# Kernel tuning notes

Measured on AMD Instinct MI355X. Metric: run time of the kernel, lower is better.

The kernel has to match this reference:

```python
import jax, jax.numpy as jnp
import numpy as np
from jax import lax

SLOPE = 0.01  # nn.LeakyReLU default negative slope

def leaky(x):
    return jnp.where(x >= 0, x, SLOPE * x)

def conv2d(x, w, b, pad):
    # x: [N,C,H,W], w: [O,I,kh,kw]
    y = lax.conv_general_dilated(x, w, (1, 1), [(pad, pad), (pad, pad)],
                                 dimension_numbers=('NCHW', 'OIHW', 'NCHW'))
    return y + b[None, :, None, None]

def centered_ifftn(x, axes):
    # np.fft.fftshift(np.fft.ifftn(np.fft.ifftshift(X), norm='ortho'))
    return jnp.fft.fftshift(jnp.fft.ifftn(jnp.fft.ifftshift(x, axes=axes), axes=axes, norm='ortho'), axes=axes)

def setup_inputs() -> dict:
    key = jax.random.key(0)
    ks = jax.random.split(key, 10)
    B, H, W, CK = 8, 640, 368, 32
    return {
        'img':    jax.random.normal(ks[0], (B, 1, H, W), jnp.float32),
        'kspace': jax.random.normal(ks[1], (B, 2, H, W), jnp.float32),
        # k_model1: Conv2d(2, CK, 3, padding=1) + LeakyReLU
        'wk': jax.random.normal(ks[2], (CK, 2, 3, 3), jnp.float32) * 0.1,
        'bk': jnp.zeros((CK,), jnp.float32),
        # conv1: Conv2d(CK, 2, kernel_size=1)
        'w1': jax.random.normal(ks[3], (2, CK, 1, 1), jnp.float32) * 0.1,
        'b1': jnp.zeros((2,), jnp.float32),
        # conv2: Conv2d(2, 1, kernel_size=1)
        'w2': jax.random.normal(ks[4], (1, 2, 1, 1), jnp.float32) * 0.1,
        'b2': jnp.zeros((1,), jnp.float32),
        # i_model1: Conv2d(1, 1, 3, padding=1) + LeakyReLU
        'wi': jax.random.normal(ks[5], (1, 1, 3, 3), jnp.float32) * 0.1,
        'bi': jnp.zeros((1,), jnp.float32),
    }

def reference(img, kspace, wk, bk, w1, b1, w2, b2, wi, bi):
    # k-space branch: k_model1 then conv1 + LeakyReLU
    out1 = leaky(conv2d(leaky(conv2d(kspace, wk, bk, 1)), w1, b1, 0))  # [B,2,H,W]
    # channel 0 = real, channel 1 = imag; ifftn over ALL axes (incl. batch),
    # exactly as the original numpy call with axes=range(out.ndim)
    cplx = out1[:, 0].astype(jnp.complex64) + 1j * out1[:, 1].astype(jnp.complex64)  # [B,H,W]
    im = jnp.abs(centered_ifftn(cplx, (0, 1, 2)))[:, None]  # [B,1,H,W]
    # concat with image, cast to half (torch.cuda.HalfTensor), conv2 + LeakyReLU
    out = jnp.concatenate([im, img], axis=1).astype(jnp.float16)  # [B,2,H,W]
    out = leaky(conv2d(out, w2.astype(jnp.float16), b2.astype(jnp.float16), 0))
    out = out.astype(jnp.float32)  # [B,1,H,W]
    # image-domain model
    return leaky(conv2d(out, wi, bi, 1))  # [B,1,H,W]
```

## Files before the change

kernel.cpp:

```cpp
#include <hip/hip_runtime.h>
#include <hip/hip_fp16.h>
#include <math.h>

#define B_ 8
#define H_ 640
#define W_ 368
#define HW_ (H_*W_)
#define NP_ (B_*H_*W_)

#define FROWS 4
#define HLINES 4
#define HP 645
#define TS 16

typedef __attribute__((ext_vector_type(8))) short v8s;
typedef __attribute__((ext_vector_type(4))) float v4f;
typedef __attribute__((ext_vector_type(16))) float v16f;

__device__ __forceinline__ float leaky_(float x){ return fmaxf(x, 0.01f*x); }

__device__ __forceinline__ unsigned short f2bf(float x){
    unsigned u = __float_as_uint(x);
    u += 0x7FFFu + ((u >> 16) & 1u);
    return (unsigned short)(u >> 16);
}

__device__ __forceinline__ float2 cadd_(float2 a, float2 b){ return make_float2(a.x+b.x, a.y+b.y); }
__device__ __forceinline__ float2 csub_(float2 a, float2 b){ return make_float2(a.x-b.x, a.y-b.y); }
__device__ __forceinline__ float2 cmul_(float2 a, float c, float s){
    return make_float2(a.x*c - a.y*s, a.x*s + a.y*c);
}
__device__ __forceinline__ float2 cmulv_(float2 a, float2 w){
    return make_float2(a.x*w.x - a.y*w.y, a.x*w.y + a.y*w.x);
}

__device__ __forceinline__ void dft4p_(float2 p0, float2 p1, float2 p2, float2 p3,
                                       float2& z0, float2& z1, float2& z2, float2& z3){
    float2 s0 = cadd_(p0,p2), d0 = csub_(p0,p2);
    float2 s1 = cadd_(p1,p3), d1 = csub_(p1,p3);
    z0 = cadd_(s0,s1);
    z2 = csub_(s0,s1);
    z1 = make_float2(d0.x - d1.y, d0.y + d1.x);
    z3 = make_float2(d0.x + d1.y, d0.y - d1.x);
}

__device__ __forceinline__ void fft16p_(const float2* x, float2* X){
    const float C1 = 0.9238795325112867f, S1 = 0.3826834323650898f;
    const float R  = 0.7071067811865476f;
    float2 Y[4][4];
    #pragma unroll
    for (int b = 0; b < 4; ++b)
        dft4p_(x[b], x[4+b], x[8+b], x[12+b], Y[b][0], Y[b][1], Y[b][2], Y[b][3]);
    Y[1][1] = cmul_(Y[1][1],  C1,  S1);
    Y[1][2] = cmul_(Y[1][2],   R,   R);
    Y[1][3] = cmul_(Y[1][3],  S1,  C1);
    Y[2][1] = cmul_(Y[2][1],   R,   R);
    Y[2][2] = make_float2(-Y[2][2].y, Y[2][2].x);
    Y[2][3] = cmul_(Y[2][3],  -R,   R);
    Y[3][1] = cmul_(Y[3][1],  S1,  C1);
    Y[3][2] = cmul_(Y[3][2],  -R,   R);
    Y[3][3] = cmul_(Y[3][3], -C1, -S1);
    #pragma unroll
    for (int c = 0; c < 4; ++c)
        dft4p_(Y[0][c], Y[1][c], Y[2][c], Y[3][c], X[c], X[c+4], X[c+8], X[c+12]);
}

__device__ __forceinline__ void fft8p_(const float2* x, float2* X){
    const float R = 0.7071067811865476f;
    float2 Y0[4], Y1[4];
    dft4p_(x[0], x[2], x[4], x[6], Y0[0], Y0[1], Y0[2], Y0[3]);
    dft4p_(x[1], x[3], x[5], x[7], Y1[0], Y1[1], Y1[2], Y1[3]);
    float2 T0 = Y1[0];
    float2 T1 = cmul_(Y1[1],  R, R);
    float2 T2 = make_float2(-Y1[2].y, Y1[2].x);
    float2 T3 = cmul_(Y1[3], -R, R);
    X[0] = cadd_(Y0[0], T0);  X[4] = csub_(Y0[0], T0);
    X[1] = cadd_(Y0[1], T1);  X[5] = csub_(Y0[1], T1);
    X[2] = cadd_(Y0[2], T2);  X[6] = csub_(Y0[2], T2);
    X[3] = cadd_(Y0[3], T3);  X[7] = csub_(Y0[3], T3);
}

__global__ void init_tables_kernel(float2* __restrict__ T){
    int i = blockIdx.x*blockDim.x + threadIdx.x;
    if (i >= 1301) return;
    int r, c, modN; int j;
    if      (i <  368){ j = i;        r = j%16; c = j/16; modN = 368; }
    else if (i < 1008){ j = i-368;    r = j%16; c = j/16; modN = 640; }
    else if (i < 1048){ j = i-1008;   r = j%8;  c = j/8;  modN = 40;  }
    else              { j = i-1048;   r = j/11; c = j%11 + 1; modN = 23; }
    int t = (int)(((long long)r * c) % modN);
    if (t > modN/2) t -= modN;
    float ang = (float)(6.283185307179586 * ((double)t / (double)modN));
    float s, co;
    sincosf(ang, &s, &co);
    T[i] = make_float2(co, s);
}

__global__ __launch_bounds__(256) void kfftw_kernel(const float* __restrict__ ksp,
                               const float* __restrict__ wk,
                               const float* __restrict__ bk,
                               const float* __restrict__ w1,
                               const float* __restrict__ b1,
                               const float2* __restrict__ TW368P,
                               const float2* __restrict__ F23P,
                               float2* __restrict__ Bt){
    __shared__ unsigned short Sb[4836];
    __shared__ float2 X[FROWS*369];
    int t = threadIdx.x;
    int blk = blockIdx.x;
    int b  = blk / 160;
    int h0 = (blk - b*160) * FROWS;

    for (int seg = 0; seg < 12; ++seg){
        int r = seg >> 1, ic = seg & 1;
        int hh = h0 - 1 + r;
        int ok = ((unsigned)hh < 640u);
        const float* base = ksp + ((size_t)(b*2 + ic)*640 + (ok ? hh : 0))*368;
        for (int col = t; col < 372; col += 256){
            int c = col - 1;
            float v = (ok && (unsigned)c < 368u) ? base[c] : 0.f;
            Sb[seg*372 + col] = f2bf(v);
        }
    }
    for (int i = t; i < 372; i += 256) Sb[4464 + i] = 0;

    int lane = t & 63, wave = t >> 6;
    int ch = lane & 31, h = lane >> 5;
    int l = wave;

    int offB[8];
    v8s a1, a2;
    #pragma unroll
    for (int j = 0; j < 8; ++j){
        int kk = 8*h + j;
        int ic = (kk >= 9) ? 1 : 0;
        int tt = kk - ic*9;
        int ty = tt/3, tx = tt - ty*3;
        offB[j] = ((ty + l)*2 + ic)*372 + tx;
        a1[j] = (short)f2bf(wk[ch*18 + kk]);
        a2[j] = 0;
    }
    if (h == 0){
        a2[0] = (short)f2bf(wk[ch*18 + 16]);
        a2[1] = (short)f2bf(wk[ch*18 + 17]);
        a2[2] = (short)f2bf(bk[ch]);
    }
    const int off16 = ((2 + l)*2 + 1)*372 + 1;
    const int off17 = off16 + 1;

    float wp0[16], wp1[16];
    #pragma unroll
    for (int r = 0; r < 16; ++r){
        int row = (r & 3) + 8*(r >> 2) + 4*h;
        wp0[r] = w1[row];
        wp1[r] = w1[32 + row];
    }
    float b10 = b1[0], b11 = b1[1];
    float sgn = (ch & 1) ? -1.f : 1.f;
    __syncthreads();

    for (int g = 0; g < 12; ++g){
        int px = g*32 + ch;
        v8s bv;
        #pragma unroll
        for (int j = 0; j < 8; ++j) bv[j] = (short)Sb[offB[j] + px];
        v16f d = {0.f,0.f,0.f,0.f,0.f,0.f,0.f,0.f,0.f,0.f,0.f,0.f,0.f,0.f,0.f,0.f};
        d = __builtin_amdgcn_mfma_f32_32x32x16_bf16(a1, bv, d, 0, 0, 0);
        v8s b2v = {0,0,0,0,0,0,0,0};
        b2v[0] = (short)Sb[off16 + px];
        b2v[1] = (short)Sb[off17 + px];
        b2v[2] = (short)0x3F80;
        d = __builtin_amdgcn_mfma_f32_32x32x16_bf16(a2, b2v, d, 0, 0, 0);
        float sx = 0.f, sy = 0.f;
        #pragma unroll
        for (int r = 0; r < 16; ++r){
            float y = leaky_(d[r]);
            sx = fmaf(y, wp0[r], sx);
            sy = fmaf(y, wp1[r], sy);
        }
        sx += __shfl_xor(sx, 32);
        sy += __shfl_xor(sy, 32);
        if (h == 0 && px < 368){
            float o0 = leaky_(sx + b10);
            float o1 = leaky_(sy + b11);
            X[l*369 + px] = make_float2(sgn*o0, sgn*o1);
        }
    }
    __syncthreads();

    if (t < 92){
        int ll = t & 3, n2 = t >> 2;
        float2 xr[16], Xo[16];
        #pragma unroll
        for (int n1 = 0; n1 < 16; ++n1) xr[n1] = X[ll*369 + 23*n1 + n2];
        fft16p_(xr, Xo);
        const float2* row = TW368P + n2*16;
        #pragma unroll
        for (int k1 = 0; k1 < 16; ++k1)
            X[ll*369 + 23*k1 + n2] = cmulv_(Xo[k1], row[k1]);
    }
    __syncthreads();

    {
        int ll = t & 3, k1 = (t >> 2) & 15, qr = t >> 6;
        const float2* xp = X + ll*369 + 23*k1;
        float2 x0 = xp[0];
        float2 u[11], d[11];
        #pragma unroll
        for (int m = 1; m <= 11; ++m){
            float2 a = xp[m], bb = xp[23-m];
            u[m-1] = cadd_(a, bb);
            d[m-1] = csub_(a, bb);
        }
        __syncthreads();
        int k2beg = qr*6;
        int k2end = (qr == 3) ? 23 : k2beg + 6;
        for (int k2 = k2beg; k2 < k2end; ++k2){
            const float2* row = F23P + k2*11;
            float re = x0.x, im = x0.y;
            #pragma unroll
            for (int m = 0; m < 11; ++m){
                float c = row[m].x, s = row[m].y;
                re += u[m].x*c - d[m].y*s;
                im += u[m].y*c + d[m].x*s;
            }
            X[ll*369 + k1 + 16*k2] = make_float2(re, im);
        }
    }
    __syncthreads();

    const float sc = 0.052129458158616354f;
    for (int i = t; i < FROWS*368; i += 256){
        int k = i >> 2, ll = i & 3;
        float2 v = X[ll*369 + k];
        float s = (k & 1) ? -sc : sc;
        Bt[((size_t)(b*368 + k))*640 + h0 + ll] = make_float2(v.x*s, v.y*s);
    }
}

__global__ __launch_bounds__(256) void fftH_kernel(const float2* __restrict__ Bt,
                                                   const float2* __restrict__ TW640P,
                                                   const float2* __restrict__ TW40P,
                                                   float2* __restrict__ A2){
    __shared__ float2 X[HLINES*HP];
    int t = threadIdx.x;
    size_t base = (size_t)blockIdx.x * (HLINES*640);

    for (int i = t; i < HLINES*640; i += 256){
        int l = i / 640, n = i - l*640;
        float2 v = Bt[base + i];
        float s = (n & 1) ? -1.f : 1.f;
        X[l*HP + n] = make_float2(v.x*s, v.y*s);
    }
    __syncthreads();

    if (t < 160){
        int l = t & 3, n2 = t >> 2;
        float2 xr[16], Xo[16];
        #pragma unroll
        for (int n1 = 0; n1 < 16; ++n1) xr[n1] = X[l*HP + 40*n1 + n2];
        fft16p_(xr, Xo);
        const float2* row = TW640P + n2*16;
        #pragma unroll
        for (int k1 = 0; k1 < 16; ++k1)
            X[l*HP + 40*k1 + n2] = cmulv_(Xo[k1], row[k1]);
    }
    __syncthreads();

    for (int it = t; it < 320; it += 256){
        int l = it & 3, k1 = (it >> 2) & 15, m2 = it >> 6;
        float2 xr[8], Xo[8];
        #pragma unroll
        for (int m1 = 0; m1 < 8; ++m1) xr[m1] = X[l*HP + 40*k1 + 5*m1 + m2];
        fft8p_(xr, Xo);
        const float2* row = TW40P + m2*8;
        #pragma unroll
        for (int j1 = 0; j1 < 8; ++j1)
            X[l*HP + 40*k1 + 5*j1 + m2] = cmulv_(Xo[j1], row[j1]);
    }
    __syncthreads();

    {
        const float CK1[5] = {1.f,  0.30901699437494745f, -0.8090169943749475f, -0.8090169943749475f,  0.30901699437494745f};
        const float SK1[5] = {0.f,  0.9510565162951535f,   0.5877852522924731f, -0.5877852522924731f, -0.9510565162951535f};
        const float CK2[5] = {1.f, -0.8090169943749475f,   0.30901699437494745f, 0.30901699437494745f, -0.8090169943749475f};
        const float SK2[5] = {0.f,  0.5877852522924731f,  -0.9510565162951535f,  0.9510565162951535f, -0.5877852522924731f};
        int it0 = t, it1 = t + 256;
        int l0 = it0 & 3, k10 = (it0 >> 2) & 15, j10 = it0 >> 6;
        int l1 = it1 & 3, k11 = (it1 >> 2) & 15, j11 = it1 >> 6;
        float2 p0[5], p1[5];
        #pragma unroll
        for (int m2 = 0; m2 < 5; ++m2) p0[m2] = X[l0*HP + 40*k10 + 5*j10 + m2];
        #pragma unroll
        for (int m2 = 0; m2 < 5; ++m2) p1[m2] = X[l1*HP + 40*k11 + 5*j11 + m2];
        __syncthreads();
        float2 u0a = cadd_(p0[1], p0[4]), d0a = csub_(p0[1], p0[4]);
        float2 u0b = cadd_(p0[2], p0[3]), d0b = csub_(p0[2], p0[3]);
        float2 u1a = cadd_(p1[1], p1[4]), d1a = csub_(p1[1], p1[4]);
        float2 u1b = cadd_(p1[2], p1[3]), d1b = csub_(p1[2], p1[3]);
        #pragma unroll
        for (int j2 = 0; j2 < 5; ++j2){
            float c1v = CK1[j2], s1v = SK1[j2], c2v = CK2[j2], s2v = SK2[j2];
            float re0 = p0[0].x + u0a.x*c1v - d0a.y*s1v + u0b.x*c2v - d0b.y*s2v;
            float im0 = p0[0].y + u0a.y*c1v + d0a.x*s1v + u0b.y*c2v + d0b.x*s2v;
            float re1 = p1[0].x + u1a.x*c1v - d1a.y*s1v + u1b.x*c2v - d1b.y*s2v;
            float im1 = p1[0].y + u1a.y*c1v + d1a.x*s1v + u1b.y*c2v + d1b.x*s2v;
            X[l0*HP + k10 + 16*j10 + 128*j2] = make_float2(re0, im0);
            X[l1*HP + k11 + 16*j11 + 128*j2] = make_float2(re1, im1);
        }
    }
    __syncthreads();

    const float sc = 0.03952847075210474f;
    for (int i = t; i < HLINES*640; i += 256){
        int l = i / 640, k = i - l*640;
        float2 v = X[l*HP + k];
        float s = (k & 1) ? -sc : sc;
        A2[base + i] = make_float2(v.x*s, v.y*s);
    }
}

__global__ __launch_bounds__(256) void tail_kernel(const float2* __restrict__ A2,
                                  const float* __restrict__ img,
                                  const float* __restrict__ w2,
                                  const float* __restrict__ b2,
                                  const float* __restrict__ wi,
                                  const float* __restrict__ bi,
                                  float* __restrict__ out){
    __shared__ float Pl[8][TS+2][TS+3];
    int t = threadIdx.x;
    int ty0 = (blockIdx.x / 23) * TS;
    int tx0 = (blockIdx.x % 23) * TS;

    float w2h0 = __half2float(__float2half(w2[0]));
    float w2h1 = __half2float(__float2half(w2[1]));
    float b2h  = __half2float(__float2half(b2[0]));
    const float sc8 = 0.35355339059327373f;

    for (int idx = t; idx < (TS+2)*(TS+2); idx += 256){
        int hx = idx / (TS+2), hy = idx - hx*(TS+2);
        int hh = ty0 - 1 + hy, ww = tx0 - 1 + hx;
        int hc = min(max(hh, 0), H_-1), wc = min(max(ww, 0), W_-1);
        float2 x[8], Xo[8];
        #pragma unroll
        for (int n = 0; n < 8; ++n){
            float2 v = A2[((size_t)(n*368 + wc))*640 + hc];
            float s = (n & 1) ? -1.f : 1.f;
            x[n] = make_float2(v.x*s, v.y*s);
        }
        fft8p_(x, Xo);
        #pragma unroll
        for (int k = 0; k < 8; ++k){
            float s = (k & 1) ? -sc8 : sc8;
            float yr = Xo[k].x * s, yi = Xo[k].y * s;
            float mag = sqrtf(yr*yr + yi*yi);
            Pl[k][hy][hx] = __half2float(__float2half(mag));
        }
    }
    __syncthreads();

    for (int idx = t; idx < (TS+2)*(TS+2); idx += 256){
        int hy = idx / (TS+2), hx = idx - hy*(TS+2);
        int hh = ty0 - 1 + hy, ww = tx0 - 1 + hx;
        bool inb = (hh >= 0) && (hh < H_) && (ww >= 0) && (ww < W_);
        int hc = min(max(hh, 0), H_-1), wc = min(max(ww, 0), W_-1);
        float inbf = inb ? 1.f : 0.f;
        #pragma unroll
        for (int k = 0; k < 8; ++k){
            float g = __half2float(__float2half(img[(size_t)k*HW_ + hc*W_ + wc]));
            float a = Pl[k][hy][hx];
            float o = leaky_(a*w2h0 + g*w2h1 + b2h);
            o = __half2float(__float2half(o));
            Pl[k][hy][hx] = o * inbf;
        }
    }
    __syncthreads();

    int sy = t >> 4, sx = t & 15;
    float wv[9];
    #pragma unroll
    for (int q = 0; q < 9; ++q) wv[q] = wi[q];
    float bi0 = bi[0];
    #pragma unroll
    for (int k = 0; k < 8; ++k){
        float acc = bi0;
        #pragma unroll
        for (int dy = 0; dy < 3; ++dy)
            #pragma unroll
            for (int dx = 0; dx < 3; ++dx)
                acc += wv[dy*3+dx] * Pl[k][sy+dy][sx+dx];
        out[((size_t)k*H_ + ty0+sy)*W_ + tx0+sx] = leaky_(acc);
    }
}

extern "C" void kernel_launch(void* const* d_in, const int* in_sizes, int n_in,
                              void* d_out, int out_size, void* d_ws, size_t ws_size,
                              hipStream_t stream){
    const float* img = (const float*)d_in[0];
    const float* ksp = (const float*)d_in[1];
    const float* wk  = (const float*)d_in[2];
    const float* bk  = (const float*)d_in[3];
    const float* w1  = (const float*)d_in[4];
    const float* b1  = (const float*)d_in[5];
    const float* w2  = (const float*)d_in[6];
    const float* b2  = (const float*)d_in[7];
    const float* wi  = (const float*)d_in[8];
    const float* bi  = (const float*)d_in[9];

    char* ws = (char*)d_ws;
    float2* Bt  = (float2*)(ws + 0);
    float2* A2  = (float2*)(ws + 15073280);
    float2* T   = (float2*)(ws + 30146560);
    float2* TW368P = T + 0;
    float2* TW640P = T + 368;
    float2* TW40P  = T + 1008;
    float2* F23P   = T + 1048;
    float* out  = (float*)d_out;

    init_tables_kernel<<<6, 256, 0, stream>>>(T);

    kfftw_kernel<<<B_*(H_/FROWS), 256, 0, stream>>>(ksp, wk, bk, w1, b1,
                                                    TW368P, F23P, Bt);
    fftH_kernel<<<(B_*W_)/HLINES, 256, 0, stream>>>(Bt, TW640P, TW40P, A2);
    tail_kernel<<<(H_/TS)*(W_/TS), 256, 0, stream>>>(A2, img, w2, b2, wi, bi, out);
}
```

Before: 155.6 us.

## Map one FFT line per wavefront and replace block barriers with compiler fences

Reassigns work in the W-direction FFT tail and the H-direction FFT kernel so each 64-lane wavefront owns one line. Block-wide __syncthreads between FFT stages become compiler-only memory fences, relying on in-wavefront lockstep execution. The H-FFT shared buffer is re-padded to one extra element every 40 to reduce bank conflicts. This removes block synchronization cost, but intra-wavefront LDS ordering without a barrier is a correctness risk, and lanes above 23 or 40 sit idle in some stages.

```diff
diff --git a/kernel.cpp b/kernel.cpp
--- a/kernel.cpp
+++ b/kernel.cpp
@@ -10,11 +10,9 @@
 
 #define FROWS 4
 #define HLINES 4
-#define HP 645
 #define TS 16
 
 typedef __attribute__((ext_vector_type(8))) short v8s;
-typedef __attribute__((ext_vector_type(4))) float v4f;
 typedef __attribute__((ext_vector_type(16))) float v16f;
 
 __device__ __forceinline__ float leaky_(float x){ return fmaxf(x, 0.01f*x); }
@@ -186,24 +184,24 @@
             X[l*369 + px] = make_float2(sgn*o0, sgn*o1);
         }
     }
-    __syncthreads();
-
-    if (t < 92){
-        int ll = t & 3, n2 = t >> 2;
+    asm volatile("" ::: "memory");
+
+    if (lane < 23){
+        int n2 = lane;
         float2 xr[16], Xo[16];
         #pragma unroll
-        for (int n1 = 0; n1 < 16; ++n1) xr[n1] = X[ll*369 + 23*n1 + n2];
+        for (int n1 = 0; n1 < 16; ++n1) xr[n1] = X[l*369 + 23*n1 + n2];
         fft16p_(xr, Xo);
         const float2* row = TW368P + n2*16;
         #pragma unroll
         for (int k1 = 0; k1 < 16; ++k1)
-            X[ll*369 + 23*k1 + n2] = cmulv_(Xo[k1], row[k1]);
-    }
-    __syncthreads();
+            X[l*369 + 23*k1 + n2] = cmulv_(Xo[k1], row[k1]);
+    }
+    asm volatile("" ::: "memory");
 
     {
-        int ll = t & 3, k1 = (t >> 2) & 15, qr = t >> 6;
-        const float2* xp = X + ll*369 + 23*k1;
+        int k1 = lane & 15, qr = lane >> 4;
+        const float2* xp = X + l*369 + 23*k1;
         float2 x0 = xp[0];
         float2 u[11], d[11];
         #pragma unroll
@@ -212,7 +210,7 @@
             u[m-1] = cadd_(a, bb);
             d[m-1] = csub_(a, bb);
         }
-        __syncthreads();
+        asm volatile("" ::: "memory");
         int k2beg = qr*6;
         int k2end = (qr == 3) ? 23 : k2beg + 6;
         for (int k2 = k2beg; k2 < k2end; ++k2){
@@ -224,7 +222,7 @@
                 re += u[m].x*c - d[m].y*s;
                 im += u[m].y*c + d[m].x*s;
             }
-            X[ll*369 + k1 + 16*k2] = make_float2(re, im);
+            X[l*369 + k1 + 16*k2] = make_float2(re, im);
         }
     }
     __syncthreads();
@@ -242,58 +240,61 @@
                                                    const float2* __restrict__ TW640P,
                                                    const float2* __restrict__ TW40P,
                                                    float2* __restrict__ A2){
-    __shared__ float2 X[HLINES*HP];
+    __shared__ float2 X[HLINES][656];
     int t = threadIdx.x;
-    size_t base = (size_t)blockIdx.x * (HLINES*640);
-
-    for (int i = t; i < HLINES*640; i += 256){
-        int l = i / 640, n = i - l*640;
-        float2 v = Bt[base + i];
+    int lane = t & 63, l = t >> 6;
+    size_t lineb = (size_t)blockIdx.x * (HLINES*640) + (size_t)l*640;
+
+    for (int n = lane; n < 640; n += 64){
+        float2 v = Bt[lineb + n];
         float s = (n & 1) ? -1.f : 1.f;
-        X[l*HP + n] = make_float2(v.x*s, v.y*s);
-    }
-    __syncthreads();
-
-    if (t < 160){
-        int l = t & 3, n2 = t >> 2;
+        X[l][n + n/40] = make_float2(v.x*s, v.y*s);
+    }
+    asm volatile("" ::: "memory");
+
+    if (lane < 40){
+        int n2 = lane;
         float2 xr[16], Xo[16];
         #pragma unroll
-        for (int n1 = 0; n1 < 16; ++n1) xr[n1] = X[l*HP + 40*n1 + n2];
+        for (int n1 = 0; n1 < 16; ++n1) xr[n1] = X[l][41*n1 + n2];
         fft16p_(xr, Xo);
         const float2* row = TW640P + n2*16;
         #pragma unroll
         for (int k1 = 0; k1 < 16; ++k1)
-            X[l*HP + 40*k1 + n2] = cmulv_(Xo[k1], row[k1]);
-    }
-    __syncthreads();
-
-    for (int it = t; it < 320; it += 256){
-        int l = it & 3, k1 = (it >> 2) & 15, m2 = it >> 6;
-        float2 xr[8], Xo[8];
-        #pragma unroll
-        for (int m1 = 0; m1 < 8; ++m1) xr[m1] = X[l*HP + 40*k1 + 5*m1 + m2];
-        fft8p_(xr, Xo);
-        const float2* row = TW40P + m2*8;
-        #pragma unroll
-        for (int j1 = 0; j1 < 8; ++j1)
-            X[l*HP + 40*k1 + 5*j1 + m2] = cmulv_(Xo[j1], row[j1]);
-    }
-    __syncthreads();
+            X[l][41*k1 + n2] = cmulv_(Xo[k1], row[k1]);
+    }
+    asm volatile("" ::: "memory");
+
+    #pragma unroll
+    for (int pass = 0; pass < 2; ++pass){
+        int it = lane + pass*64;
+        if (it < 80){
+            int k1 = it & 15, m2 = it >> 4;
+            float2 xr[8], Xo[8];
+            #pragma unroll
+            for (int m1 = 0; m1 < 8; ++m1) xr[m1] = X[l][41*k1 + 5*m1 + m2];
+            fft8p_(xr, Xo);
+            const float2* row = TW40P + m2*8;
+            #pragma unroll
+            for (int j1 = 0; j1 < 8; ++j1)
+                X[l][41*k1 + 5*j1 + m2] = cmulv_(Xo[j1], row[j1]);
+        }
+    }
+    asm volatile("" ::: "memory");
 
     {
         const float CK1[5] = {1.f,  0.30901699437494745f, -0.8090169943749475f, -0.8090169943749475f,  0.30901699437494745f};
         const float SK1[5] = {0.f,  0.9510565162951535f,   0.5877852522924731f, -0.5877852522924731f, -0.9510565162951535f};
         const float CK2[5] = {1.f, -0.8090169943749475f,   0.30901699437494745f, 0.30901699437494745f, -0.8090169943749475f};
         const float SK2[5] = {0.f,  0.5877852522924731f,  -0.9510565162951535f,  0.9510565162951535f, -0.5877852522924731f};
-        int it0 = t, it1 = t + 256;
-        int l0 = it0 & 3, k10 = (it0 >> 2) & 15, j10 = it0 >> 6;
-        int l1 = it1 & 3, k11 = (it1 >> 2) & 15, j11 = it1 >> 6;
+        int k10 = lane & 15, j10 = lane >> 4;
+        int j11 = j10 + 4;
         float2 p0[5], p1[5];
         #pragma unroll
-        for (int m2 = 0; m2 < 5; ++m2) p0[m2] = X[l0*HP + 40*k10 + 5*j10 + m2];
-        #pragma unroll
-        for (int m2 = 0; m2 < 5; ++m2) p1[m2] = X[l1*HP + 40*k11 + 5*j11 + m2];
-        __syncthreads();
+        for (int m2 = 0; m2 < 5; ++m2) p0[m2] = X[l][41*k10 + 5*j10 + m2];
+        #pragma unroll
+        for (int m2 = 0; m2 < 5; ++m2) p1[m2] = X[l][41*k10 + 5*j11 + m2];
+        asm volatile("" ::: "memory");
         float2 u0a = cadd_(p0[1], p0[4]), d0a = csub_(p0[1], p0[4]);
         float2 u0b = cadd_(p0[2], p0[3]), d0b = csub_(p0[2], p0[3]);
         float2 u1a = cadd_(p1[1], p1[4]), d1a = csub_(p1[1], p1[4]);
@@ -305,18 +306,19 @@
             float im0 = p0[0].y + u0a.y*c1v + d0a.x*s1v + u0b.y*c2v + d0b.x*s2v;
             float re1 = p1[0].x + u1a.x*c1v - d1a.y*s1v + u1b.x*c2v - d1b.y*s2v;
             float im1 = p1[0].y + u1a.y*c1v + d1a.x*s1v + u1b.y*c2v + d1b.x*s2v;
-            X[l0*HP + k10 + 16*j10 + 128*j2] = make_float2(re0, im0);
-            X[l1*HP + k11 + 16*j11 + 128*j2] = make_float2(re1, im1);
-        }
-    }
-    __syncthreads();
+            int ka = k10 + 16*j10 + 128*j2;
+            int kb = k10 + 16*j11 + 128*j2;
+            X[l][ka + ka/40] = make_float2(re0, im0);
+            X[l][kb + kb/40] = make_float2(re1, im1);
+        }
+    }
+    asm volatile("" ::: "memory");
 
     const float sc = 0.03952847075210474f;
-    for (int i = t; i < HLINES*640; i += 256){
-        int l = i / 640, k = i - l*640;
-        float2 v = X[l*HP + k];
+    for (int k = lane; k < 640; k += 64){
+        float2 v = X[l][k + k/40];
         float s = (k & 1) ? -sc : sc;
-        A2[base + i] = make_float2(v.x*s, v.y*s);
+        A2[lineb + k] = make_float2(v.x*s, v.y*s);
     }
 }
 
```

After: 156.9 us. About the same (+0.8%).

## Load kspace directly from global and make row FFT stages wave-local

Applied to the files above, without the earlier changes.

The bf16 LDS staging of the kspace halo is removed. Each lane now reads its conv inputs directly from global memory, with clamped addresses and masks, and converts them to bf16 in registers. The row FFT stages are remapped so each wave handles its own row. The block-wide barriers are replaced with compiler memory fences on the assumption that the work is wave-local. This cuts the staging pass and the barriers, but adds redundant global loads (about 9x reuse that now goes through cache) and relies on in-wave LDS ordering for correctness.

```diff
diff --git a/kernel.cpp b/kernel.cpp
--- a/kernel.cpp
+++ b/kernel.cpp
@@ -14,7 +14,6 @@
 #define TS 16
 
 typedef __attribute__((ext_vector_type(8))) short v8s;
-typedef __attribute__((ext_vector_type(4))) float v4f;
 typedef __attribute__((ext_vector_type(16))) float v16f;
 
 __device__ __forceinline__ float leaky_(float x){ return fmaxf(x, 0.01f*x); }
@@ -104,31 +103,18 @@
                                const float2* __restrict__ TW368P,
                                const float2* __restrict__ F23P,
                                float2* __restrict__ Bt){
-    __shared__ unsigned short Sb[4836];
     __shared__ float2 X[FROWS*369];
     int t = threadIdx.x;
     int blk = blockIdx.x;
     int b  = blk / 160;
     int h0 = (blk - b*160) * FROWS;
 
-    for (int seg = 0; seg < 12; ++seg){
-        int r = seg >> 1, ic = seg & 1;
-        int hh = h0 - 1 + r;
-        int ok = ((unsigned)hh < 640u);
-        const float* base = ksp + ((size_t)(b*2 + ic)*640 + (ok ? hh : 0))*368;
-        for (int col = t; col < 372; col += 256){
-            int c = col - 1;
-            float v = (ok && (unsigned)c < 368u) ? base[c] : 0.f;
-            Sb[seg*372 + col] = f2bf(v);
-        }
-    }
-    for (int i = t; i < 372; i += 256) Sb[4464 + i] = 0;
-
     int lane = t & 63, wave = t >> 6;
     int ch = lane & 31, h = lane >> 5;
     int l = wave;
 
-    int offB[8];
+    int off[8], cbv[8];
+    float mskf[8];
     v8s a1, a2;
     #pragma unroll
     for (int j = 0; j < 8; ++j){
@@ -136,7 +122,11 @@
         int ic = (kk >= 9) ? 1 : 0;
         int tt = kk - ic*9;
         int ty = tt/3, tx = tt - ty*3;
-        offB[j] = ((ty + l)*2 + ic)*372 + tx;
+        int row = h0 + l - 1 + ty;
+        mskf[j] = ((unsigned)row < 640u) ? 1.f : 0.f;
+        int rowc = min(max(row, 0), 639);
+        off[j] = ((b*2 + ic)*640 + rowc)*368;
+        cbv[j] = tx - 1;
         a1[j] = (short)f2bf(wk[ch*18 + kk]);
         a2[j] = 0;
     }
@@ -145,8 +135,9 @@
         a2[1] = (short)f2bf(wk[ch*18 + 17]);
         a2[2] = (short)f2bf(bk[ch]);
     }
-    const int off16 = ((2 + l)*2 + 1)*372 + 1;
-    const int off17 = off16 + 1;
+    int row16 = h0 + l + 1;
+    float m16 = ((unsigned)row16 < 640u) ? 1.f : 0.f;
+    int off16 = ((b*2 + 1)*640 + min(row16, 639))*368;
 
     float wp0[16], wp1[16];
     #pragma unroll
@@ -157,18 +148,27 @@
     }
     float b10 = b1[0], b11 = b1[1];
     float sgn = (ch & 1) ? -1.f : 1.f;
-    __syncthreads();
 
     for (int g = 0; g < 12; ++g){
         int px = g*32 + ch;
         v8s bv;
         #pragma unroll
-        for (int j = 0; j < 8; ++j) bv[j] = (short)Sb[offB[j] + px];
+        for (int j = 0; j < 8; ++j){
+            int col  = px + cbv[j];
+            int colc = min(max(col, 0), 367);
+            float ldv = ksp[off[j] + colc];
+            float v = (col == colc) ? ldv * mskf[j] : 0.f;
+            bv[j] = (short)f2bf(v);
+        }
         v16f d = {0.f,0.f,0.f,0.f,0.f,0.f,0.f,0.f,0.f,0.f,0.f,0.f,0.f,0.f,0.f,0.f};
         d = __builtin_amdgcn_mfma_f32_32x32x16_bf16(a1, bv, d, 0, 0, 0);
+        int c16 = min(px, 367);
+        int c17 = min(px + 1, 367);
+        float v16 = ((px     < 368) ? ksp[off16 + c16] : 0.f) * m16;
+        float v17 = ((px + 1 < 368) ? ksp[off16 + c17] : 0.f) * m16;
         v8s b2v = {0,0,0,0,0,0,0,0};
-        b2v[0] = (short)Sb[off16 + px];
-        b2v[1] = (short)Sb[off17 + px];
+        b2v[0] = (short)f2bf(v16);
+        b2v[1] = (short)f2bf(v17);
         b2v[2] = (short)0x3F80;
         d = __builtin_amdgcn_mfma_f32_32x32x16_bf16(a2, b2v, d, 0, 0, 0);
         float sx = 0.f, sy = 0.f;
@@ -186,24 +186,24 @@
             X[l*369 + px] = make_float2(sgn*o0, sgn*o1);
         }
     }
-    __syncthreads();
-
-    if (t < 92){
-        int ll = t & 3, n2 = t >> 2;
+    asm volatile("" ::: "memory");
+
+    if (lane < 23){
+        int n2 = lane;
         float2 xr[16], Xo[16];
         #pragma unroll
-        for (int n1 = 0; n1 < 16; ++n1) xr[n1] = X[ll*369 + 23*n1 + n2];
+        for (int n1 = 0; n1 < 16; ++n1) xr[n1] = X[l*369 + 23*n1 + n2];
         fft16p_(xr, Xo);
         const float2* row = TW368P + n2*16;
         #pragma unroll
         for (int k1 = 0; k1 < 16; ++k1)
-            X[ll*369 + 23*k1 + n2] = cmulv_(Xo[k1], row[k1]);
-    }
-    __syncthreads();
+            X[l*369 + 23*k1 + n2] = cmulv_(Xo[k1], row[k1]);
+    }
+    asm volatile("" ::: "memory");
 
     {
-        int ll = t & 3, k1 = (t >> 2) & 15, qr = t >> 6;
-        const float2* xp = X + ll*369 + 23*k1;
+        int k1 = lane & 15, qr = lane >> 4;
+        const float2* xp = X + l*369 + 23*k1;
         float2 x0 = xp[0];
         float2 u[11], d[11];
         #pragma unroll
@@ -212,7 +212,7 @@
             u[m-1] = cadd_(a, bb);
             d[m-1] = csub_(a, bb);
         }
-        __syncthreads();
+        asm volatile("" ::: "memory");
         int k2beg = qr*6;
         int k2end = (qr == 3) ? 23 : k2beg + 6;
         for (int k2 = k2beg; k2 < k2end; ++k2){
@@ -224,7 +224,7 @@
                 re += u[m].x*c - d[m].y*s;
                 im += u[m].y*c + d[m].x*s;
             }
-            X[ll*369 + k1 + 16*k2] = make_float2(re, im);
+            X[l*369 + k1 + 16*k2] = make_float2(re, im);
         }
     }
     __syncthreads();
```

Result: slower. 187.3 us (+20.4%).

## Assign one wavefront per row in W-FFT and move transpose into H-FFT load

Applied to the files above, without the earlier changes.

The W-direction FFT stages in kfftw_kernel now give each of the four wavefronts its own row, so block-wide __syncthreads between stages become compiler memory barriers. The intermediate buffer is written row-major (unstrided) instead of being transposed on store. fftH_kernel now does the transpose on its load side, reading 4 adjacent columns per row with short strided reads. This trades scattered stores in the first kernel for partially coalesced gathers in the second, and relies on wavefront-synchronous LDS access being safe without barriers.

```diff
diff --git a/kernel.cpp b/kernel.cpp
--- a/kernel.cpp
+++ b/kernel.cpp
@@ -14,7 +14,6 @@
 #define TS 16
 
 typedef __attribute__((ext_vector_type(8))) short v8s;
-typedef __attribute__((ext_vector_type(4))) float v4f;
 typedef __attribute__((ext_vector_type(16))) float v16f;
 
 __device__ __forceinline__ float leaky_(float x){ return fmaxf(x, 0.01f*x); }
@@ -186,24 +185,24 @@
             X[l*369 + px] = make_float2(sgn*o0, sgn*o1);
         }
     }
-    __syncthreads();
-
-    if (t < 92){
-        int ll = t & 3, n2 = t >> 2;
+    asm volatile("" ::: "memory");
+
+    if (lane < 23){
+        int n2 = lane;
         float2 xr[16], Xo[16];
         #pragma unroll
-        for (int n1 = 0; n1 < 16; ++n1) xr[n1] = X[ll*369 + 23*n1 + n2];
+        for (int n1 = 0; n1 < 16; ++n1) xr[n1] = X[l*369 + 23*n1 + n2];
         fft16p_(xr, Xo);
         const float2* row = TW368P + n2*16;
         #pragma unroll
         for (int k1 = 0; k1 < 16; ++k1)
-            X[ll*369 + 23*k1 + n2] = cmulv_(Xo[k1], row[k1]);
-    }
-    __syncthreads();
+            X[l*369 + 23*k1 + n2] = cmulv_(Xo[k1], row[k1]);
+    }
+    asm volatile("" ::: "memory");
 
     {
-        int ll = t & 3, k1 = (t >> 2) & 15, qr = t >> 6;
-        const float2* xp = X + ll*369 + 23*k1;
+        int k1 = lane & 15, qr = lane >> 4;
+        const float2* xp = X + l*369 + 23*k1;
         float2 x0 = xp[0];
         float2 u[11], d[11];
         #pragma unroll
@@ -212,7 +211,7 @@
             u[m-1] = cadd_(a, bb);
             d[m-1] = csub_(a, bb);
         }
-        __syncthreads();
+        asm volatile("" ::: "memory");
         int k2beg = qr*6;
         int k2end = (qr == 3) ? 23 : k2beg + 6;
         for (int k2 = k2beg; k2 < k2end; ++k2){
@@ -224,17 +223,17 @@
                 re += u[m].x*c - d[m].y*s;
                 im += u[m].y*c + d[m].x*s;
             }
-            X[ll*369 + k1 + 16*k2] = make_float2(re, im);
+            X[l*369 + k1 + 16*k2] = make_float2(re, im);
         }
     }
     __syncthreads();
 
     const float sc = 0.052129458158616354f;
     for (int i = t; i < FROWS*368; i += 256){
-        int k = i >> 2, ll = i & 3;
+        int ll = i / 368, k = i - ll*368;
         float2 v = X[ll*369 + k];
         float s = (k & 1) ? -sc : sc;
-        Bt[((size_t)(b*368 + k))*640 + h0 + ll] = make_float2(v.x*s, v.y*s);
+        Bt[((size_t)(b*640 + h0 + ll))*368 + k] = make_float2(v.x*s, v.y*s);
     }
 }
 
@@ -244,13 +243,15 @@
                                                    float2* __restrict__ A2){
     __shared__ float2 X[HLINES*HP];
     int t = threadIdx.x;
-    size_t base = (size_t)blockIdx.x * (HLINES*640);
+    int b  = blockIdx.x / 92;
+    int w0 = (blockIdx.x - b*92) * HLINES;
+    size_t inb = (size_t)b * 640 * 368 + w0;
 
     for (int i = t; i < HLINES*640; i += 256){
-        int l = i / 640, n = i - l*640;
-        float2 v = Bt[base + i];
-        float s = (n & 1) ? -1.f : 1.f;
-        X[l*HP + n] = make_float2(v.x*s, v.y*s);
+        int h = i >> 2, ws = i & 3;
+        float2 v = Bt[inb + (size_t)h*368 + ws];
+        float s = (h & 1) ? -1.f : 1.f;
+        X[ws*HP + h] = make_float2(v.x*s, v.y*s);
     }
     __syncthreads();
 
@@ -312,11 +313,12 @@
     __syncthreads();
 
     const float sc = 0.03952847075210474f;
+    size_t outb = ((size_t)b*368 + w0)*640;
     for (int i = t; i < HLINES*640; i += 256){
         int l = i / 640, k = i - l*640;
         float2 v = X[l*HP + k];
         float s = (k & 1) ? -sc : sc;
-        A2[base + i] = make_float2(v.x*s, v.y*s);
+        A2[outb + i] = make_float2(v.x*s, v.y*s);
     }
 }
 
@@ -421,6 +423,6 @@
 
     kfftw_kernel<<<B_*(H_/FROWS), 256, 0, stream>>>(ksp, wk, bk, w1, b1,
                                                     TW368P, F23P, Bt);
-    fftH_kernel<<<(B_*W_)/HLINES, 256, 0, stream>>>(Bt, TW640P, TW40P, A2);
+    fftH_kernel<<<8*92, 256, 0, stream>>>(Bt, TW640P, TW40P, A2);
     tail_kernel<<<(H_/TS)*(W_/TS), 256, 0, stream>>>(A2, img, w2, b2, wi, bi, out);
 }
```

Measured after the change: 158.1 us. Within noise of the previous version (+1.6%).
